# Kernel tuning notes

Hardware: AMD Instinct MI355X
Metric: run time of the kernel (lower is better)

## Reference

```python
import jax, jax.numpy as jnp
import numpy as np
from jax import lax

B = 32; C_IN = 3; HW = 64
CL1_F = 64; CL1_K = 5
V = 1024
CL2_F = 128; CL2_K = 16
CL3_F = 256; CL3_K = 16
FC1_F = 512; FC2_F = 10
FC1_IN = CL3_F * (V // 16)  # 16384


def _sym_laplacian(k, v):
    # symmetric, spectral norm < 1 (mimics rescaled Laplacian 2L/lmax - I spectrum)
    a = jax.random.normal(k, (v, v), jnp.float32) / np.float32(np.sqrt(v))
    return (a + a.T) * jnp.float32(0.3)


def setup_inputs():
    key = jax.random.key(0)
    ks = jax.random.split(key, 10)
    def n(k, shape, s):
        return jax.random.normal(k, shape, jnp.float32) * jnp.float32(s)
    x = jax.random.normal(ks[0], (B, C_IN, HW, HW), jnp.float32)
    conv1_w = n(ks[1], (CL1_F, C_IN, CL1_K, CL1_K), 0.05)
    conv1_b = jnp.zeros((CL1_F,), jnp.float32)
    L1 = _sym_laplacian(ks[2], V)
    L2 = _sym_laplacian(ks[3], V // 4)
    g = HW // 2  # pooled grid side = 32
    ii, jj = jnp.meshgrid(jnp.arange(g), jnp.arange(g), indexing='ij')
    node_index = jnp.stack([ii.reshape(-1), jj.reshape(-1)], axis=1).astype(jnp.int32)  # [V,2]
    perm = jnp.arange(V, dtype=jnp.int32)
    k2_w = n(ks[4], (CL2_F, CL1_F * CL2_K), 0.04)
    k2_b = jnp.zeros((CL2_F,), jnp.float32)
    k3_w = n(ks[5], (CL3_F, CL2_F * CL3_K), 0.03)
    k3_b = jnp.zeros((CL3_F,), jnp.float32)
    fc1_w = n(ks[6], (FC1_F, FC1_IN), 0.01)
    fc1_b = jnp.zeros((FC1_F,), jnp.float32)
    fc2_w = n(ks[7], (FC2_F, FC1_F), 0.05)
    fc2_b = jnp.zeros((FC2_F,), jnp.float32)
    return {"x": x, "conv1_w": conv1_w, "conv1_b": conv1_b, "L1": L1, "L2": L2,
            "node_index": node_index, "perm": perm,
            "k2_w": k2_w, "k2_b": k2_b, "k3_w": k3_w, "k3_b": k3_b,
            "fc1_w": fc1_w, "fc1_b": fc1_b, "fc2_w": fc2_w, "fc2_b": fc2_b}


def _graph_conv(x, L, W, b, K):
    # x: (B, C, V). Chebyshev basis T_k(L) x, then linear over (C*K).
    Bb, C, Vv = x.shape
    x0 = jnp.transpose(x, (2, 1, 0)).reshape(Vv, C * Bb)  # [V, C*B]
    xs = [x0, L @ x0]
    for _ in range(K - 2):
        xs.append(2.0 * (L @ xs[-1]) - xs[-2])
    xk = jnp.stack(xs, axis=0).reshape(K, Vv, C, Bb)  # [K,V,C,B]
    xk = jnp.transpose(xk, (3, 1, 2, 0)).reshape(Bb * Vv, C * K)  # [B*V, C*K]
    out = xk @ W.T + b  # [B*V, Fout]
    return jnp.transpose(out.reshape(Bb, Vv, -1), (0, 2, 1))  # (B, Fout, V)


def reference(x, conv1_w, conv1_b, L1, L2, node_index, perm,
              k2_w, k2_b, k3_w, k3_b, fc1_w, fc1_b, fc2_w, fc2_b):
    pad = (CL1_K - 1) // 2
    y = lax.conv_general_dilated(x, conv1_w, (1, 1), [(pad, pad), (pad, pad)],
                                 dimension_numbers=('NCHW', 'OIHW', 'NCHW'))
    y = jax.nn.relu(y + conv1_b[None, :, None, None])
    Bb, C, H, Wd = y.shape
    y = y.reshape(Bb, C, H // 2, 2, Wd // 2, 2).max(axis=(3, 5))  # MaxPool2d(2,2)
    y = y[:, :, node_index[:, 0], node_index[:, 1]]  # (B, C, V)
    y = y[:, :, perm]
    # BatchNorm1d(affine=False), training-mode batch stats, biased variance
    mean = y.mean(axis=(0, 2), keepdims=True)
    var = y.var(axis=(0, 2), keepdims=True)
    y = (y - mean) * lax.rsqrt(var + 1e-5)
    y = jax.nn.relu(_graph_conv(y, L1, k2_w, k2_b, CL2_K))
    y = y.reshape(Bb, CL2_F, -1, 4).max(axis=-1)  # Graph_MaxPool(4)
    y = jax.nn.relu(_graph_conv(y, L2, k3_w, k3_b, CL3_K))
    y = y.reshape(Bb, CL3_F, -1, 4).max(axis=-1)
    y = y.reshape(Bb, FC1_IN)
    y = jax.nn.relu(y @ fc1_w.T + fc1_b)  # dropout p=0 -> identity
    return y @ fc2_w.T + fc2_b
```

## Files before the change

### kernel.cpp

```cpp
#include <hip/hip_runtime.h>
#include <hip/hip_bf16.h>

#define BB 32
#define C_IN 3
#define HW 64
#define V1 1024
#define CL2_F 128
#define V2 256
#define CL3_F 256
#define FC1_IN 16384

typedef unsigned short ushortT;
typedef __attribute__((ext_vector_type(8))) short bf16x8;
typedef __attribute__((ext_vector_type(8))) unsigned short u16x8;
typedef __attribute__((ext_vector_type(4))) float f32x4;

__device__ __forceinline__ float bfu2f(unsigned short u) {
  union { unsigned int i; float f; } x; x.i = ((unsigned)u) << 16; return x.f;
}
__device__ __forceinline__ unsigned short f2bf(float v) {
  union { float f; unsigned int i; } x; x.f = v;
  unsigned r = x.i + 0x7FFFu + ((x.i >> 16) & 1u);
  return (unsigned short)(r >> 16);
}
__device__ __forceinline__ void gload16(const ushortT* g, ushortT* l) {
  __builtin_amdgcn_global_load_lds((const __attribute__((address_space(1))) void*)g,
                                   (__attribute__((address_space(3))) void*)l, 16, 0, 0);
}

__global__ __launch_bounds__(256) void conv_pool_k(const float* __restrict__ x,
                                                   const float* __restrict__ w,
                                                   const float* __restrict__ bias,
                                                   float* __restrict__ P) {
  __shared__ float xs[3][7][72];
  __shared__ float wl[64][76];
  const int b = blockIdx.x >> 5, ph = blockIdx.x & 31;
  const int t = threadIdx.x;
  for (int i = t; i < 64 * 75; i += 256) wl[i / 75][i % 75] = w[i];
  for (int i = t; i < 3 * 7 * 72; i += 256) {
    int col = i % 72, rr = (i / 72) % 7, ci = i / (72 * 7);
    int ih = 2 * ph - 2 + rr, iw = col - 2;
    float v = 0.f;
    if (ih >= 0 && ih < HW && iw >= 0 && iw < HW)
      v = x[((b * 3 + ci) * HW + ih) * HW + iw];
    xs[ci][rr][col] = v;
  }
  __syncthreads();
  const int co = t >> 2, pq = t & 3;
  float acc[8][2][2];
#pragma unroll
  for (int i = 0; i < 8; ++i)
#pragma unroll
    for (int a = 0; a < 2; ++a)
#pragma unroll
      for (int d = 0; d < 2; ++d) acc[i][a][d] = 0.f;
  for (int ci = 0; ci < 3; ++ci) {
#pragma unroll
    for (int kh = 0; kh < 5; ++kh) {
      float w5[5];
#pragma unroll
      for (int j = 0; j < 5; ++j) w5[j] = wl[co][ci * 25 + kh * 5 + j];
#pragma unroll
      for (int dy = 0; dy < 2; ++dy) {
        const int r = kh + dy;
        float in[20];
#pragma unroll
        for (int q4 = 0; q4 < 5; ++q4) {
          float4 v4 = *(const float4*)&xs[ci][r][16 * pq + q4 * 4];
          in[q4 * 4 + 0] = v4.x; in[q4 * 4 + 1] = v4.y;
          in[q4 * 4 + 2] = v4.z; in[q4 * 4 + 3] = v4.w;
        }
#pragma unroll
        for (int i = 0; i < 8; ++i)
#pragma unroll
          for (int dx = 0; dx < 2; ++dx)
#pragma unroll
            for (int kw = 0; kw < 5; ++kw)
              acc[i][dy][dx] += w5[kw] * in[2 * i + dx + kw];
      }
    }
  }
  const float bv = bias[co];
#pragma unroll
  for (int i = 0; i < 8; ++i) {
    float m = fmaxf(fmaxf(acc[i][0][0], acc[i][0][1]), fmaxf(acc[i][1][0], acc[i][1][1]));
    P[((size_t)(b * 64 + co) << 10) + (ph << 5) + pq * 8 + i] = fmaxf(m + bv, 0.f);
  }
}

__global__ __launch_bounds__(256) void bn_part_k(const float* __restrict__ P,
                                                 float* __restrict__ buf) {
  int c = blockIdx.x, s = blockIdx.y;
  float s1 = 0.f, s2 = 0.f;
  for (int i = threadIdx.x; i < 4096; i += 256) {
    int b = s * 4 + (i >> 10), p = i & 1023;
    float v = P[((size_t)(b * 64 + c) << 10) + p];
    s1 += v; s2 += v * v;
  }
#pragma unroll
  for (int o = 32; o > 0; o >>= 1) { s1 += __shfl_down(s1, o); s2 += __shfl_down(s2, o); }
  __shared__ float sh[2][4];
  int wid = threadIdx.x >> 6;
  if ((threadIdx.x & 63) == 0) { sh[0][wid] = s1; sh[1][wid] = s2; }
  __syncthreads();
  if (threadIdx.x == 0) {
    buf[c * 8 + s] = sh[0][0] + sh[0][1] + sh[0][2] + sh[0][3];
    buf[512 + c * 8 + s] = sh[1][0] + sh[1][1] + sh[1][2] + sh[1][3];
  }
}
__global__ __launch_bounds__(64) void bn_comb_k(float* __restrict__ buf) {
  int c = threadIdx.x;
  float s1 = 0.f, s2 = 0.f;
#pragma unroll
  for (int s = 0; s < 8; ++s) { s1 += buf[c * 8 + s]; s2 += buf[512 + c * 8 + s]; }
  float mean = s1 / 32768.f;
  float var = s2 / 32768.f - mean * mean;
  buf[1024 + c] = mean;
  buf[1088 + c] = rsqrtf(var + 1e-5f);
}

__global__ __launch_bounds__(256) void build_x0_k(const float* __restrict__ P,
                                                  const float* __restrict__ buf,
                                                  const int* __restrict__ ni,
                                                  const int* __restrict__ perm,
                                                  ushortT* __restrict__ PGh,
                                                  ushortT* __restrict__ PGl,
                                                  ushortT* __restrict__ CW0) {
  __shared__ float vals[64][33];
  __shared__ int qv[32];
  const int b = blockIdx.x >> 5, vc = blockIdx.x & 31;
  const int t = threadIdx.x;
  if (t < 32) {
    int pv = perm[vc * 32 + t];
    qv[t] = ni[2 * pv] * 32 + ni[2 * pv + 1];
  }
  __syncthreads();
  {
    int c = t & 63, vh = t >> 6;
    float mean = buf[1024 + c], rstd = buf[1088 + c];
    const float* pc = &P[((size_t)(b * 64 + c)) << 10];
#pragma unroll
    for (int j = 0; j < 8; ++j) {
      int vl = vh * 8 + j;
      vals[c][vl] = (pc[qv[vl]] - mean) * rstd;
    }
  }
  __syncthreads();
  {
    int c = t & 63, vo = t >> 6;
    u16x8 h8, l8;
#pragma unroll
    for (int j = 0; j < 8; ++j) {
      float f = vals[c][vo * 8 + j];
      unsigned short h = f2bf(f);
      h8[j] = h; l8[j] = f2bf(f - bfu2f(h));
    }
    size_t base = ((size_t)(vc * 4 + vo) * 2048 + b * 64 + c) * 8;
    *(u16x8*)&PGh[base] = h8;
    *(u16x8*)&PGl[base] = l8;
  }
  {
    int co = t & 7, vl = t >> 3;
    u16x8 h8;
#pragma unroll
    for (int j = 0; j < 8; ++j) h8[j] = f2bf(vals[co * 8 + j][vl]);
    *(u16x8*)&CW0[((size_t)co * 32768 + b * 1024 + vc * 32 + vl) * 8] = h8;
  }
}

__global__ __launch_bounds__(256) void lsplit_k(const float* __restrict__ L,
                                                ushortT* __restrict__ Lh,
                                                ushortT* __restrict__ Ll, int V) {
  int id = blockIdx.x * 256 + threadIdx.x;
  int n = id & (V - 1), koct = id / V * 8;
  u16x8 h8, l8;
#pragma unroll
  for (int j = 0; j < 8; ++j) {
    float v = L[(size_t)(koct + j) * V + n];
    unsigned short h = f2bf(v);
    h8[j] = h; l8[j] = f2bf(v - bfu2f(h));
  }
  size_t o = (size_t)id * 8;
  *(u16x8*)&Lh[o] = h8;
  *(u16x8*)&Ll[o] = l8;
}

__global__ __launch_bounds__(256) void wprep_k(const float* __restrict__ W,
                                               ushortT* __restrict__ WAh,
                                               ushortT* __restrict__ WAl, int Cc, int Nf) {
  int d = blockIdx.x * 256 + threadIdx.x;
  if (d >= Nf * 16 * Cc) return;
  int j = d & 7;
  int f = (d >> 3) % Nf;
  int koct = d / (8 * Nf);
  int k = koct * 8 + j;
  int kq = k / Cc, c = k % Cc;
  float v = W[(size_t)f * (Cc * 16) + c * 16 + kq];
  unsigned short h = f2bf(v);
  WAh[d] = h; WAl[d] = f2bf(v - bfu2f(h));
}

template <int MODE, int SWZ, int KD>
__global__ __launch_bounds__(256) void cheb_step_k(
    int Mld, int mt,
    const ushortT* __restrict__ Ah, const ushortT* __restrict__ Al,
    const ushortT* __restrict__ Lbh, const ushortT* __restrict__ Lbl,
    ushortT* __restrict__ Ph, ushortT* __restrict__ Pl,
    ushortT* __restrict__ CW, int CB, int CSH) {
  constexpr int NPH = KD / 64;
  __shared__ ushortT sA[3][2][8][520];
  int bx, by;
  if (SWZ) {
    const int id = blockIdx.x;
    const int xcd = id & 7, pos = id >> 3;
    bx = (xcd & 3) * 8 + (pos & 7);
    by = (xcd >> 2) * 8 + (pos >> 3);
  } else {
    bx = blockIdx.x % mt;
    by = blockIdx.x / mt;
  }
  const int m0 = bx * 64, n0 = by * 64;
  const int t = threadIdx.x, lane = t & 63;
  const int wr = (t >> 6) >> 1, wc = (t >> 6) & 1;
  const int lm = lane & 15, lq = lane >> 4;
  const size_t bCol = (size_t)(n0 + wc * 32 + lm);

  f32x4 acc[2][2];
#pragma unroll
  for (int mi = 0; mi < 2; ++mi)
#pragma unroll
    for (int nj = 0; nj < 2; ++nj) acc[mi][nj] = (f32x4){0.f, 0.f, 0.f, 0.f};

  bf16x8 Bh[2][2][2], Bl[2][2][2];

#define STAGEA(buf, slot)                                                          \
  {                                                                                \
    const int koct = (slot) * 8;                                                   \
    _Pragma("unroll") for (int i = 0; i < 2; ++i) {                                \
      const int sl = (t + i * 256) >> 6;                                           \
      const int ln = t & 63;                                                       \
      const size_t ga = ((size_t)(koct + sl) * Mld + m0 + ln) * 8;                 \
      gload16(Ah + ga, &sA[buf][0][sl][0]);                                        \
      gload16(Al + ga, &sA[buf][1][sl][0]);                                        \
    }                                                                              \
  }

#define LOADB(set, slot)                                                           \
  {                                                                                \
    _Pragma("unroll") for (int ks = 0; ks < 2; ++ks)                               \
        _Pragma("unroll") for (int nj = 0; nj < 2; ++nj) {                         \
      size_t o = ((size_t)((slot) * 8 + ks * 4 + lq) * KD + bCol + nj * 16) * 8;   \
      Bh[set][ks][nj] = *(const bf16x8*)(Lbh + o);                                 \
      Bl[set][ks][nj] = *(const bf16x8*)(Lbl + o);                                 \
    }                                                                              \
  }

#define DOMFMA(buf, set)                                                           \
  {                                                                                \
    _Pragma("unroll") for (int ks = 0; ks < 2; ++ks) {                             \
      const int so = ks * 4 + lq;                                                  \
      bf16x8 xah[2], xal[2];                                                       \
      _Pragma("unroll") for (int mi = 0; mi < 2; ++mi) {                           \
        const int r = (wr * 32 + mi * 16 + lm) * 8;                                \
        xah[mi] = *(const bf16x8*)&sA[buf][0][so][r];                              \
        xal[mi] = *(const bf16x8*)&sA[buf][1][so][r];                              \
      }                                                                            \
      _Pragma("unroll") for (int mi = 0; mi < 2; ++mi)                             \
          _Pragma("unroll") for (int nj = 0; nj < 2; ++nj) {                       \
        acc[mi][nj] = __builtin_amdgcn_mfma_f32_16x16x32_bf16(xah[mi], Bh[set][ks][nj], \
                                                              acc[mi][nj], 0, 0, 0);\
        acc[mi][nj] = __builtin_amdgcn_mfma_f32_16x16x32_bf16(xal[mi], Bh[set][ks][nj], \
                                                              acc[mi][nj], 0, 0, 0);\
        acc[mi][nj] = __builtin_amdgcn_mfma_f32_16x16x32_bf16(xah[mi], Bl[set][ks][nj], \
                                                              acc[mi][nj], 0, 0, 0);\
      }                                                                            \
    }                                                                              \
  }

  STAGEA(0, 0);
  STAGEA(1, 1);
  LOADB(0, 0);
#pragma unroll
  for (int tt = 0; tt < NPH; ++tt) {
    asm volatile("s_waitcnt vmcnt(12) lgkmcnt(0)" ::: "memory");
    __builtin_amdgcn_s_barrier();
    STAGEA((tt + 2) % 3, (tt + 2) % NPH);
    LOADB((tt + 1) % 2, (tt + 1) % NPH);
    __builtin_amdgcn_s_setprio(1);
    DOMFMA(tt % 3, tt % 2);
    __builtin_amdgcn_s_setprio(0);
  }
  asm volatile("s_waitcnt vmcnt(0)" ::: "memory");
  __syncthreads();
#undef STAGEA
#undef LOADB
#undef DOMFMA

  float* fs = (float*)&sA[0][0][0][0];
#pragma unroll
  for (int mi = 0; mi < 2; ++mi)
#pragma unroll
    for (int nj = 0; nj < 2; ++nj)
#pragma unroll
      for (int j = 0; j < 4; ++j) {
        int gm_l = wr * 32 + mi * 16 + lq * 4 + j;
        int gn_l = wc * 32 + nj * 16 + lm;
        fs[gm_l * 65 + gn_l] = acc[mi][nj][j];
      }
  __syncthreads();

  const size_t noct0 = (size_t)(n0 >> 3);
#pragma unroll
  for (int r = 0; r < 2; ++r) {
    int id = t + r * 256;
    int gm_l = id >> 3, go = id & 7;
    size_t g = ((noct0 + go) * Mld + (m0 + gm_l)) * 8;
    float nv[8];
#pragma unroll
    for (int i = 0; i < 8; ++i) nv[i] = fs[gm_l * 65 + go * 8 + i];
    if (MODE == 1) {
      u16x8 ph = *(const u16x8*)&Ph[g];
      u16x8 pl = *(const u16x8*)&Pl[g];
#pragma unroll
      for (int i = 0; i < 8; ++i) nv[i] = 2.f * nv[i] - (bfu2f(ph[i]) + bfu2f(pl[i]));
    }
    u16x8 h8, l8;
#pragma unroll
    for (int i = 0; i < 8; ++i) {
      unsigned short h = f2bf(nv[i]);
      h8[i] = h; l8[i] = f2bf(nv[i] - bfu2f(h));
    }
    *(u16x8*)&Ph[g] = h8;
    *(u16x8*)&Pl[g] = l8;
    if (MODE == 1) {
#pragma unroll
      for (int i = 0; i < 8; ++i) fs[gm_l * 65 + go * 8 + i] = nv[i];
    }
  }
  __syncthreads();

  const int cBase = m0 & (CB - 1);
  const int bidx = m0 >> CSH;
  const size_t NNs = (size_t)KD << 5;
#pragma unroll
  for (int r = 0; r < 2; ++r) {
    int id = t + r * 256;
    int gn_l = id & 63, coI = id >> 6;
    u16x8 h8;
#pragma unroll
    for (int i = 0; i < 8; ++i) h8[i] = f2bf(fs[(coI * 8 + i) * 65 + gn_l]);
    size_t cbase = ((size_t)((cBase >> 3) + coI) * NNs + (size_t)bidx * KD + n0 + gn_l) * 8;
    *(u16x8*)&CW[cbase] = h8;
  }
}

template <int Cc, int NSPL>
__global__ __launch_bounds__(256) void wapply_k(
    int NN, int Nf,
    const ushortT* __restrict__ WAh, const ushortT* __restrict__ WAl,
    const ushortT* __restrict__ cwBase, size_t cwN,
    float* __restrict__ OUT, size_t outStride) {
  constexpr int S = Cc / 2;
  constexpr int SPZ = S / NSPL;
  constexpr int ROWU = 129 * 8;
  __shared__ ushortT sX[3][4 * ROWU];
  const int z = blockIdx.z;
  OUT += (size_t)z * outStride;
  const int m0 = blockIdx.x * 64, n0 = blockIdx.y * 128;
  const int t = threadIdx.x, lane = t & 63, wid = t >> 6;
  const int wr = wid >> 1, wc = wid & 1;
  const int lm = lane & 15, lq = lane >> 4;

  const int fIdx = m0 + wr * 32 + lm;
  const int s0 = z * SPZ;

  f32x4 acc[2][4];
#pragma unroll
  for (int mi = 0; mi < 2; ++mi)
#pragma unroll
    for (int nj = 0; nj < 4; ++nj) acc[mi][nj] = (f32x4){0.f, 0.f, 0.f, 0.f};

  bf16x8 wh[2][2], wl[2][2];

#define STX(buf, s)                                                                \
  {                                                                                \
    const int buf_ = (Cc == 64) ? ((s) >> 1) : ((s) >> 2);                         \
    const int lo_ = (Cc == 64) ? (((s) & 1) * 4) : (((s) & 3) * 4);                \
    const ushortT* xb_ = cwBase + (size_t)buf_ * cwN;                              \
    _Pragma("unroll") for (int i = 0; i < 2; ++i) {                                \
      const int idx = t + i * 256;                                                 \
      const int octrow = idx >> 7, col = idx & 127;                                \
      const int chunk = idx >> 6;                                                  \
      const ushortT* src = xb_ + ((size_t)(lo_ + octrow) * NN + n0 + col) * 8;     \
      gload16(src, &sX[buf][octrow * ROWU + (chunk & 1) * 512]);                   \
    }                                                                              \
  }

#define LDW(set, s)                                                                \
  {                                                                                \
    _Pragma("unroll") for (int mi = 0; mi < 2; ++mi) {                             \
      size_t o = ((size_t)((s)*4 + lq) * Nf + fIdx + mi * 16) * 8;                 \
      wh[set][mi] = *(const bf16x8*)(WAh + o);                                     \
      wl[set][mi] = *(const bf16x8*)(WAl + o);                                     \
    }                                                                              \
  }

#define XMFMA(buf, set)                                                            \
  {                                                                                \
    bf16x8 xf[4];                                                                  \
    _Pragma("unroll") for (int nj = 0; nj < 4; ++nj)                               \
        xf[nj] = *(const bf16x8*)&sX[buf][lq * ROWU + (wc * 64 + lm + nj * 16) * 8];\
    _Pragma("unroll") for (int mi = 0; mi < 2; ++mi)                               \
        _Pragma("unroll") for (int nj = 0; nj < 4; ++nj) {                         \
      acc[mi][nj] = __builtin_amdgcn_mfma_f32_16x16x32_bf16(wh[set][mi], xf[nj],   \
                                                            acc[mi][nj], 0, 0, 0); \
      acc[mi][nj] = __builtin_amdgcn_mfma_f32_16x16x32_bf16(wl[set][mi], xf[nj],   \
                                                            acc[mi][nj], 0, 0, 0); \
    }                                                                              \
  }

  STX(0, s0);
  STX(1, s0 + 1);
  LDW(0, s0);
#pragma unroll
  for (int tt = 0; tt < SPZ; ++tt) {
    asm volatile("s_waitcnt vmcnt(6) lgkmcnt(0)" ::: "memory");
    __builtin_amdgcn_s_barrier();
    STX((tt + 2) % 3, s0 + (tt + 2) % SPZ);
    LDW((tt + 1) % 2, s0 + (tt + 1) % SPZ);
    __builtin_amdgcn_s_setprio(1);
    XMFMA(tt % 3, tt % 2);
    __builtin_amdgcn_s_setprio(0);
  }
#undef STX
#undef LDW
#undef XMFMA

#pragma unroll
  for (int mi = 0; mi < 2; ++mi)
#pragma unroll
    for (int nj = 0; nj < 4; ++nj)
#pragma unroll
      for (int j = 0; j < 4; ++j) {
        int gm = m0 + wr * 32 + mi * 16 + lq * 4 + j;
        int gn = n0 + wc * 64 + nj * 16 + lm;
        OUT[(size_t)gm * NN + gn] = acc[mi][nj][j];
      }
}

__global__ __launch_bounds__(256) void relu_pool1_k(const float* __restrict__ OUT1P,
                                                    const float* __restrict__ b2,
                                                    ushortT* __restrict__ PG2h,
                                                    ushortT* __restrict__ PG2l,
                                                    ushortT* __restrict__ CW0) {
  __shared__ float sval[128][9];
  const int b = blockIdx.x >> 5, vc = blockIdx.x & 31;
  const int t = threadIdx.x;
  const size_t PS = (size_t)128 * 32768;
  {
    int f = t & 127, h = t >> 7;
    float bb = b2[f];
    const float* src = &OUT1P[(size_t)f * 32768 + b * 1024 + vc * 32];
#pragma unroll
    for (int i = 0; i < 4; ++i) {
      int v2l = h * 4 + i;
      float4 r0 = *(const float4*)&src[v2l * 4];
      float4 r1 = *(const float4*)&src[PS + v2l * 4];
      float s0 = r0.x + r1.x, s1 = r0.y + r1.y, s2 = r0.z + r1.z, s3 = r0.w + r1.w;
      float m = fmaxf(fmaxf(s0, s1), fmaxf(s2, s3));
      sval[f][v2l] = fmaxf(m + bb, 0.f);
    }
  }
  __syncthreads();
  if (t < 128) {
    int f = t;
    u16x8 h8, l8;
#pragma unroll
    for (int j = 0; j < 8; ++j) {
      float v = sval[f][j];
      unsigned short h = f2bf(v);
      h8[j] = h; l8[j] = f2bf(v - bfu2f(h));
    }
    size_t base = ((size_t)vc * 4096 + b * 128 + f) * 8;
    *(u16x8*)&PG2h[base] = h8;
    *(u16x8*)&PG2l[base] = l8;
  } else {
    int q = t - 128;
    int co = q & 15, v2l = q >> 4;
    u16x8 h8;
#pragma unroll
    for (int j = 0; j < 8; ++j) h8[j] = f2bf(sval[co * 8 + j][v2l]);
    *(u16x8*)&CW0[((size_t)co * 8192 + b * 256 + vc * 8 + v2l) * 8] = h8;
  }
}

__global__ __launch_bounds__(256) void relu_pool2_k(const float* __restrict__ OUT2P,
                                                    const float* __restrict__ b3,
                                                    float* __restrict__ At) {
  int n = blockIdx.x * 256 + threadIdx.x;
  int v3 = n & 63, f = (n >> 6) & 255, b = n >> 14;
  const size_t PS = (size_t)256 * 8192;
  size_t base = ((size_t)f * 32 + b) * 256 + v3 * 4;
  float4 r0 = *(const float4*)&OUT2P[base];
  float4 r1 = *(const float4*)&OUT2P[PS + base];
  float4 r2 = *(const float4*)&OUT2P[2 * PS + base];
  float4 r3 = *(const float4*)&OUT2P[3 * PS + base];
  float s0 = r0.x + r1.x + r2.x + r3.x;
  float s1 = r0.y + r1.y + r2.y + r3.y;
  float s2 = r0.z + r1.z + r2.z + r3.z;
  float s3 = r0.w + r1.w + r2.w + r3.w;
  float m = fmaxf(fmaxf(s0, s1), fmaxf(s2, s3));
  At[(size_t)b * FC1_IN + f * 64 + v3] = fmaxf(m + b3[f], 0.f);
}

__global__ __launch_bounds__(256) void fc1_part_k(const float* __restrict__ At,
                                                  const float* __restrict__ W1,
                                                  float* __restrict__ part) {
  __shared__ float sWt[64][68];
  __shared__ float sA[64][33];
  const int jt = blockIdx.x, ks = blockIdx.y;
  const int j0 = jt * 64, kb = ks * 512;
  const int t = threadIdx.x;
  const int b = t & 31, jg = t >> 5;
  float acc[8] = {};
  for (int k0 = kb; k0 < kb + 512; k0 += 64) {
    __syncthreads();
    {
      int jr = t >> 2, kq = t & 3;
      const float* wp = &W1[(size_t)(j0 + jr) * FC1_IN + k0 + kq * 16];
#pragma unroll
      for (int i = 0; i < 4; ++i) {
        float4 w4 = *(const float4*)(wp + 4 * i);
        int kk = kq * 16 + 4 * i;
        sWt[kk + 0][jr] = w4.x; sWt[kk + 1][jr] = w4.y;
        sWt[kk + 2][jr] = w4.z; sWt[kk + 3][jr] = w4.w;
      }
    }
    {
      int br = t >> 3, ko = t & 7;
      const float* ap = &At[(size_t)br * FC1_IN + k0 + ko * 8];
      float4 a0 = *(const float4*)ap;
      float4 a1 = *(const float4*)(ap + 4);
      int kk = ko * 8;
      sA[kk + 0][br] = a0.x; sA[kk + 1][br] = a0.y; sA[kk + 2][br] = a0.z; sA[kk + 3][br] = a0.w;
      sA[kk + 4][br] = a1.x; sA[kk + 5][br] = a1.y; sA[kk + 6][br] = a1.z; sA[kk + 7][br] = a1.w;
    }
    __syncthreads();
#pragma unroll 8
    for (int kk = 0; kk < 64; ++kk) {
      float a = sA[kk][b];
      float wv[8];
      *(float4*)wv = *(const float4*)&sWt[kk][jg * 8];
      *(float4*)(wv + 4) = *(const float4*)&sWt[kk][jg * 8 + 4];
#pragma unroll
      for (int i = 0; i < 8; ++i) acc[i] += wv[i] * a;
    }
  }
#pragma unroll
  for (int i = 0; i < 8; ++i)
    part[((size_t)ks * 512 + j0 + jg * 8 + i) * 32 + b] = acc[i];
}

__global__ __launch_bounds__(256) void fc1_combine_k(const float* __restrict__ part,
                                                     const float* __restrict__ b1,
                                                     float* __restrict__ h) {
  int n = blockIdx.x * 256 + threadIdx.x;
  int b = n >> 9, j = n & 511;
  float s = b1[j];
#pragma unroll
  for (int ks = 0; ks < 32; ++ks) s += part[((size_t)ks * 512 + j) * 32 + b];
  h[n] = fmaxf(s, 0.f);
}

__global__ __launch_bounds__(64) void fc2_k(const float* __restrict__ h,
                                            const float* __restrict__ W2,
                                            const float* __restrict__ b2f,
                                            float* __restrict__ out) {
  int n = blockIdx.x * 64 + threadIdx.x;
  if (n >= 320) return;
  int b = n / 10, o = n % 10;
  float s = b2f[o];
  const float* hp = h + b * 512;
  const float* wp = W2 + o * 512;
  for (int j = 0; j < 512; ++j) s += hp[j] * wp[j];
  out[n] = s;
}

extern "C" void kernel_launch(void* const* d_in, const int* in_sizes, int n_in,
                              void* d_out, int out_size, void* d_ws, size_t ws_size,
                              hipStream_t stream) {
  const float* x      = (const float*)d_in[0];
  const float* conv1w = (const float*)d_in[1];
  const float* conv1b = (const float*)d_in[2];
  const float* L1     = (const float*)d_in[3];
  const float* L2     = (const float*)d_in[4];
  const int*   ni     = (const int*)d_in[5];
  const int*   perm   = (const int*)d_in[6];
  const float* k2w    = (const float*)d_in[7];
  const float* k2b    = (const float*)d_in[8];
  const float* k3w    = (const float*)d_in[9];
  const float* k3b    = (const float*)d_in[10];
  const float* fc1w   = (const float*)d_in[11];
  const float* fc1b   = (const float*)d_in[12];
  const float* fc2w   = (const float*)d_in[13];
  const float* fc2b   = (const float*)d_in[14];
  float* out = (float*)d_out;

  char* ws = (char*)d_ws;
  const size_t MB = 1024 * 1024;
  float*   P    = (float*)(ws + 0);
  ushortT* cw1  = (ushortT*)(ws + 8 * MB);
  const size_t CW1N = 2u * 1024 * 1024;
  ushortT* pgAh = (ushortT*)(ws + 72 * MB);
  ushortT* pgAl = (ushortT*)(ws + 76 * MB);
  ushortT* pgBh = (ushortT*)(ws + 80 * MB);
  ushortT* pgBl = (ushortT*)(ws + 84 * MB);
  float*   OUT1P = (float*)(ws + 88 * MB);
  ushortT* L1h  = (ushortT*)(ws + 121 * MB);
  ushortT* L1l  = (ushortT*)(ws + 123 * MB);
  ushortT* WA1h = (ushortT*)(ws + 125 * MB);
  ushortT* WA1l = (ushortT*)(ws + 125 * MB + 262144);
  float*   BNB  = (float*)(ws + 126 * MB);
  ushortT* cw2  = (ushortT*)(ws + 0);
  const size_t CW2N = 1024u * 1024;
  ushortT* pg2Ah = (ushortT*)(ws + 32 * MB);
  ushortT* pg2Al = (ushortT*)(ws + 34 * MB);
  ushortT* pg2Bh = (ushortT*)(ws + 36 * MB);
  ushortT* pg2Bl = (ushortT*)(ws + 38 * MB);
  float*   OUT2P = (float*)(ws + 40 * MB);
  ushortT* L2h  = (ushortT*)(ws + 73 * MB);
  ushortT* L2l  = (ushortT*)(ws + 73 * MB + 131072);
  ushortT* WA2h = (ushortT*)(ws + 74 * MB);
  ushortT* WA2l = (ushortT*)(ws + 75 * MB);
  float*   At   = (float*)(ws + 76 * MB);
  float*   PART = (float*)(ws + 78 * MB);
  float*   H    = (float*)(ws + 80 * MB);

  conv_pool_k<<<1024, 256, 0, stream>>>(x, conv1w, conv1b, P);
  bn_part_k<<<dim3(64, 8), 256, 0, stream>>>(P, BNB);
  bn_comb_k<<<1, 64, 0, stream>>>(BNB);
  lsplit_k<<<512, 256, 0, stream>>>(L1, L1h, L1l, 1024);
  wprep_k<<<512, 256, 0, stream>>>(k2w, WA1h, WA1l, 64, 128);
  build_x0_k<<<1024, 256, 0, stream>>>(P, BNB, ni, perm, pgAh, pgAl, cw1 + 0 * CW1N);

  cheb_step_k<0, 1, 1024><<<512, 256, 0, stream>>>(2048, 32, pgAh, pgAl, L1h, L1l,
                                                   pgBh, pgBl, cw1 + 1 * CW1N, 64, 6);
  for (int k = 2; k < 16; ++k) {
    ushortT *ah, *al, *oh, *ol;
    if (k & 1) { ah = pgAh; al = pgAl; oh = pgBh; ol = pgBl; }
    else       { ah = pgBh; al = pgBl; oh = pgAh; ol = pgAl; }
    cheb_step_k<1, 1, 1024><<<512, 256, 0, stream>>>(2048, 32, ah, al, L1h, L1l,
                                                     oh, ol, cw1 + (size_t)k * CW1N, 64, 6);
  }
  wapply_k<64, 2><<<dim3(2, 256, 2), 256, 0, stream>>>(32768, 128, WA1h, WA1l,
                                                       cw1, CW1N, OUT1P, (size_t)128 * 32768);

  relu_pool1_k<<<1024, 256, 0, stream>>>(OUT1P, k2b, pg2Ah, pg2Al, cw2 + 0 * CW2N);
  lsplit_k<<<32, 256, 0, stream>>>(L2, L2h, L2l, 256);
  wprep_k<<<2048, 256, 0, stream>>>(k3w, WA2h, WA2l, 128, 256);

  cheb_step_k<0, 0, 256><<<256, 256, 0, stream>>>(4096, 64, pg2Ah, pg2Al, L2h, L2l,
                                                  pg2Bh, pg2Bl, cw2 + 1 * CW2N, 128, 7);
  for (int k = 2; k < 16; ++k) {
    ushortT *ah, *al, *oh, *ol;
    if (k & 1) { ah = pg2Ah; al = pg2Al; oh = pg2Bh; ol = pg2Bl; }
    else       { ah = pg2Bh; al = pg2Bl; oh = pg2Ah; ol = pg2Al; }
    cheb_step_k<1, 0, 256><<<256, 256, 0, stream>>>(4096, 64, ah, al, L2h, L2l,
                                                    oh, ol, cw2 + (size_t)k * CW2N, 128, 7);
  }
  wapply_k<128, 4><<<dim3(4, 64, 4), 256, 0, stream>>>(8192, 256, WA2h, WA2l,
                                                       cw2, CW2N, OUT2P, (size_t)256 * 8192);

  relu_pool2_k<<<2048, 256, 0, stream>>>(OUT2P, k3b, At);
  fc1_part_k<<<dim3(8, 32), 256, 0, stream>>>(At, fc1w, PART);
  fc1_combine_k<<<64, 256, 0, stream>>>(PART, fc1b, H);
  fc2_k<<<5, 64, 0, stream>>>(H, fc2w, fc2b, out);
}
```

Before: 570.7 us.

## Fuse second-layer Chebyshev recurrence into one persistent LDS-resident slab kernel

```diff
diff --git a/kernel.cpp b/kernel.cpp
--- a/kernel.cpp
+++ b/kernel.cpp
@@ -354,6 +354,83 @@
   }
 }
 
+__global__ __launch_bounds__(256) void cheb2_slab_k(
+    const ushortT* __restrict__ PG2h, const ushortT* __restrict__ PG2l,
+    const ushortT* __restrict__ Lbh, const ushortT* __restrict__ Lbl,
+    ushortT* __restrict__ cw, size_t cwN) {
+  __shared__ ushortT stH[2][16][33 * 8];
+  __shared__ ushortT stL[2][16][33 * 8];
+  const int m0 = blockIdx.x * 16;
+  const int t = threadIdx.x, lane = t & 63, w = t >> 6;
+  const int lm = lane & 15, lq = lane >> 4;
+  const int n0w = w * 64;
+
+  for (int i = t; i < 16 * 32; i += 256) {
+    int m = i >> 5, voct = i & 31;
+    size_t g = ((size_t)voct * 4096 + m0 + m) * 8;
+    *(u16x8*)&stH[0][m][voct * 8] = *(const u16x8*)&PG2h[g];
+    *(u16x8*)&stL[0][m][voct * 8] = *(const u16x8*)&PG2l[g];
+  }
+  __syncthreads();
+
+  const int cb = (m0 & 127) >> 3;
+  const int bi = m0 >> 7;
+
+#pragma unroll 1
+  for (int k = 1; k < 16; ++k) {
+    const int sa = (k + 1) & 1;
+    const int sw = k & 1;
+    f32x4 acc[4];
+#pragma unroll
+    for (int nj = 0; nj < 4; ++nj) acc[nj] = (f32x4){0.f, 0.f, 0.f, 0.f};
+
+#pragma unroll
+    for (int ks = 0; ks < 8; ++ks) {
+      const int koct = ks * 4 + lq;
+      bf16x8 ah = *(const bf16x8*)&stH[sa][lm][koct * 8];
+      bf16x8 al = *(const bf16x8*)&stL[sa][lm][koct * 8];
+#pragma unroll
+      for (int nj = 0; nj < 4; ++nj) {
+        size_t o = ((size_t)koct * 256 + n0w + nj * 16 + lm) * 8;
+        bf16x8 bh = *(const bf16x8*)(Lbh + o);
+        bf16x8 bl = *(const bf16x8*)(Lbl + o);
+        acc[nj] = __builtin_amdgcn_mfma_f32_16x16x32_bf16(ah, bh, acc[nj], 0, 0, 0);
+        acc[nj] = __builtin_amdgcn_mfma_f32_16x16x32_bf16(al, bh, acc[nj], 0, 0, 0);
+        acc[nj] = __builtin_amdgcn_mfma_f32_16x16x32_bf16(ah, bl, acc[nj], 0, 0, 0);
+      }
+    }
+
+#pragma unroll
+    for (int nj = 0; nj < 4; ++nj) {
+      int n = n0w + nj * 16 + lm;
+      int vo8 = (n >> 3) * 8 + (n & 7);
+#pragma unroll
+      for (int j = 0; j < 4; ++j) {
+        int m = lq * 4 + j;
+        float d = acc[nj][j];
+        float nv;
+        if (k > 1) nv = 2.f * d - (bfu2f(stH[sw][m][vo8]) + bfu2f(stL[sw][m][vo8]));
+        else nv = d;
+        unsigned short h = f2bf(nv);
+        stH[sw][m][vo8] = h;
+        stL[sw][m][vo8] = f2bf(nv - bfu2f(h));
+      }
+    }
+    __syncthreads();
+
+    ushortT* CWk = cw + (size_t)k * cwN;
+#pragma unroll
+    for (int r = 0; r < 2; ++r) {
+      int id = t + r * 256;
+      int fo = id >> 8, v = id & 255;
+      u16x8 h8;
+#pragma unroll
+      for (int j = 0; j < 8; ++j) h8[j] = stH[sw][fo * 8 + j][(v >> 3) * 8 + (v & 7)];
+      *(u16x8*)&CWk[((size_t)(cb + fo) * 8192 + (size_t)bi * 256 + v) * 8] = h8;
+    }
+  }
+}
+
 template <int Cc, int NSPL>
 __global__ __launch_bounds__(256) void wapply_k(
     int NN, int Nf,
@@ -625,8 +702,6 @@
   const size_t CW2N = 1024u * 1024;
   ushortT* pg2Ah = (ushortT*)(ws + 32 * MB);
   ushortT* pg2Al = (ushortT*)(ws + 34 * MB);
-  ushortT* pg2Bh = (ushortT*)(ws + 36 * MB);
-  ushortT* pg2Bl = (ushortT*)(ws + 38 * MB);
   float*   OUT2P = (float*)(ws + 40 * MB);
   ushortT* L2h  = (ushortT*)(ws + 73 * MB);
   ushortT* L2l  = (ushortT*)(ws + 73 * MB + 131072);
@@ -659,15 +734,8 @@
   lsplit_k<<<32, 256, 0, stream>>>(L2, L2h, L2l, 256);
   wprep_k<<<2048, 256, 0, stream>>>(k3w, WA2h, WA2l, 128, 256);
 
-  cheb_step_k<0, 0, 256><<<256, 256, 0, stream>>>(4096, 64, pg2Ah, pg2Al, L2h, L2l,
-                                                  pg2Bh, pg2Bl, cw2 + 1 * CW2N, 128, 7);
-  for (int k = 2; k < 16; ++k) {
-    ushortT *ah, *al, *oh, *ol;
-    if (k & 1) { ah = pg2Ah; al = pg2Al; oh = pg2Bh; ol = pg2Bl; }
-    else       { ah = pg2Bh; al = pg2Bl; oh = pg2Ah; ol = pg2Al; }
-    cheb_step_k<1, 0, 256><<<256, 256, 0, stream>>>(4096, 64, ah, al, L2h, L2l,
-                                                    oh, ol, cw2 + (size_t)k * CW2N, 128, 7);
-  }
+  cheb2_slab_k<<<256, 256, 0, stream>>>(pg2Ah, pg2Al, L2h, L2l, cw2, CW2N);
+
   wapply_k<128, 4><<<dim3(4, 64, 4), 256, 0, stream>>>(8192, 256, WA2h, WA2l,
                                                        cw2, CW2N, OUT2P, (size_t)256 * 8192);
 
```

Measured after the change: 517.1 us. 1.1x faster.
